# Kernel optimization log

Hardware: AMD Instinct MI355X
Metric: run time of the kernel (lower is better)

Reference implementation:

```python
import jax, jax.numpy as jnp
import numpy as np

V = 50000
E = 800000
B, FIN, FOUT, K = 2, 64, 64, 4


def setup_inputs() -> dict:
    key = jax.random.key(0)
    k1, k2, k3, k4, k5, k6 = jax.random.split(key, 6)
    inputs = jax.random.normal(k1, (B, V, FIN), dtype=jnp.float32)
    weight = jax.random.normal(k2, (K, FIN, FOUT), dtype=jnp.float32) * np.sqrt(2.0 / (FIN * K)).astype(np.float32)
    bias = jax.random.normal(k3, (FOUT,), dtype=jnp.float32)
    lap_vals = jax.random.normal(k4, (E,), dtype=jnp.float32)
    lap_rows = jax.random.randint(k5, (E,), 0, V, dtype=jnp.int32)
    lap_cols = jax.random.randint(k6, (E,), 0, V, dtype=jnp.int32)
    return {"inputs": inputs, "weight": weight, "bias": bias,
            "lap_vals": lap_vals, "lap_rows": lap_rows, "lap_cols": lap_cols}


def reference(inputs, weight, bias, lap_vals, lap_rows, lap_cols):
    B_, V_, Fin = inputs.shape
    K_, _, Fout = weight.shape

    def spmm(x):  # L @ x, L in COO; x: [V, Fin*B]
        return jax.ops.segment_sum(lap_vals[:, None] * x[lap_cols], lap_rows, num_segments=V_)

    # x0: [V, Fin*B] (Fin-major flatten, matching torch permute(1,2,0).view)
    x0 = jnp.transpose(inputs, (1, 2, 0)).reshape(V_, Fin * B_)
    xs = [x0]
    if K_ > 1:
        x1 = spmm(x0)
        xs.append(x1)
        for _ in range(2, K_):
            x2 = 2.0 * spmm(x1) - x0
            xs.append(x2)
            x0, x1 = x1, x2
    # [K,V,Fin,B] -> [B,V,Fin,K] -> [B*V, Fin*K]
    X = jnp.stack(xs).reshape(K_, V_, Fin, B_)
    X = jnp.transpose(X, (3, 1, 2, 0)).reshape(B_ * V_, Fin * K_)
    # faithful to original: weight flattened as (K*Fin, Fout)
    out = X @ weight.reshape(K_ * Fin, Fout)
    return out.reshape(B_, V_, Fout) + bias
```

## Files before the change

### kernel.cpp

```cpp
#include <hip/hip_runtime.h>
#include <hip/hip_bf16.h>


#define NV 50000
#define NE 800000
#define XROW 128
#define NROWS 100000
#define NTILES 6250
#define EPMAX 1600000
#define BSHIFT 7
#define RPB 128
#define NB 391
#define CAP 3072
#define CHUNK 4096
#define P1_BLOCKS 196
#define X0_BLOCKS 12500

using u16 = unsigned short;
using u32 = unsigned int;
using u64 = unsigned long long;
typedef __bf16 bf16x8 __attribute__((ext_vector_type(8)));
typedef float f32x4 __attribute__((ext_vector_type(4)));

__device__ __forceinline__ float bflo(u32 g) { return __uint_as_float(g << 16); }
__device__ __forceinline__ float bfhi(u32 g) { return __uint_as_float(g & 0xffff0000u); }
__device__ __forceinline__ u32 pack_bf2(float a, float b) {
    u16 ha = __builtin_bit_cast(u16, (__bf16)a);
    u16 hb = __builtin_bit_cast(u16, (__bf16)b);
    return (u32)ha | ((u32)hb << 16);
}
__device__ __forceinline__ float unpack_f16hi(u32 rec) {
    u16 h = (u16)(rec >> 16);
    return (float)__builtin_bit_cast(_Float16, h);
}
__device__ __forceinline__ int pad16(int n) { return (n + 15) & ~15; }

__global__ __launch_bounds__(256) void bin1_k(const int* __restrict__ rows, const int* __restrict__ cols,
                                              const float* __restrict__ vals,
                                              int* __restrict__ binctr, u64* __restrict__ tmp) {
    __shared__ int bcnt[NB];
    __shared__ int bofs[NB];
    __shared__ int bcur[NB];
    __shared__ int gbase[NB];
    __shared__ int ps[256];
    __shared__ u64 stage[CHUNK];
    int t = threadIdx.x;
    int base = blockIdx.x * CHUNK;
    int n = NE - base;
    if (n > CHUNK) n = CHUNK;
    if (n <= 0) return;

    for (int i = t; i < NB; i += 256) bcnt[i] = 0;
    __syncthreads();

    for (int i = t; i < n; i += 256) {
        atomicAdd(&bcnt[rows[base + i] >> BSHIFT], 1);
    }
    __syncthreads();

    int i0 = 2 * t, i1 = 2 * t + 1;
    int a0 = (i0 < NB) ? bcnt[i0] : 0;
    int a1 = (i1 < NB) ? bcnt[i1] : 0;
    ps[t] = a0 + a1;
    __syncthreads();
    for (int off = 1; off < 256; off <<= 1) {
        int v = (t >= off) ? ps[t - off] : 0;
        __syncthreads();
        ps[t] += v;
        __syncthreads();
    }
    int eb = ps[t] - (a0 + a1);
    if (i0 < NB) { bofs[i0] = eb;      bcur[i0] = eb;      gbase[i0] = i0 * CAP + atomicAdd(&binctr[i0], a0); }
    if (i1 < NB) { bofs[i1] = eb + a0; bcur[i1] = eb + a0; gbase[i1] = i1 * CAP + atomicAdd(&binctr[i1], a1); }
    __syncthreads();

    for (int i = t; i < n; i += 256) {
        int r = rows[base + i];
        int c = cols[base + i];
        u16 hv = __builtin_bit_cast(u16, (_Float16)vals[base + i]);
        u64 rec = ((u64)(u32)r << 32) | (u64)((u32)c | ((u32)hv << 16));
        int s = atomicAdd(&bcur[r >> BSHIFT], 1);
        stage[s] = rec;
    }
    __syncthreads();

    for (int i = t; i < n; i += 256) {
        u64 rec = stage[i];
        int b = (int)(rec >> (32 + BSHIFT));
        tmp[(size_t)(gbase[b] + (i - bofs[b]))] = rec;
    }
}

__global__ __launch_bounds__(256) void bcnt_k(const u64* __restrict__ tmp, const int* __restrict__ binctr,
                                              int* __restrict__ rowc, int* __restrict__ btot,
                                              int* __restrict__ done,
                                              int* __restrict__ bbase, int* __restrict__ row_ptr) {
    __shared__ int rc[RPB];
    __shared__ int rs[RPB];
    __shared__ int ps[256];
    __shared__ int flag;
    int b = blockIdx.x, t = threadIdx.x;
    int n = binctr[b];
    const u64* rec = tmp + (size_t)b * CAP;
    if (t < RPB) rc[t] = 0;
    __syncthreads();
    for (int i = t; i < n; i += 256) {
        atomicAdd(&rc[(int)(rec[i] >> 32) & (RPB - 1)], 1);
    }
    __syncthreads();
    if (t < RPB) {
        rowc[b * RPB + t] = rc[t];
        rs[t] = pad16(rc[t]);
    }
    __syncthreads();
    for (int off = 64; off > 0; off >>= 1) {
        if (t < off) rs[t] += rs[t + off];
        __syncthreads();
    }
    if (t == 0) {
        btot[b] = rs[0];
        __threadfence();
        int ticket = atomicAdd(done, 1);
        flag = (ticket == NB - 1);
    }
    __syncthreads();
    if (flag) {
        __threadfence();
        int i0 = 2 * t, i1 = 2 * t + 1;
        int a0 = (i0 < NB) ? atomicAdd(&btot[i0], 0) : 0;
        int a1 = (i1 < NB) ? atomicAdd(&btot[i1], 0) : 0;
        ps[t] = a0 + a1;
        __syncthreads();
        for (int off = 1; off < 256; off <<= 1) {
            int v = (t >= off) ? ps[t - off] : 0;
            __syncthreads();
            ps[t] += v;
            __syncthreads();
        }
        int eb = ps[t] - (a0 + a1);
        if (i0 < NB) bbase[i0] = eb;
        if (i1 < NB) bbase[i1] = eb + a0;
        if (t == 255) row_ptr[NV] = ps[255];
    }
}

__global__ __launch_bounds__(256) void place_k(const u64* __restrict__ tmp, const int* __restrict__ binctr,
                                               const int* __restrict__ rowc, const int* __restrict__ bbase,
                                               int* __restrict__ row_ptr, u32* __restrict__ epack) {
    __shared__ int rc[RPB];
    __shared__ int ro[RPB];
    int b = blockIdx.x, t = threadIdx.x;
    int n = binctr[b];
    int base = bbase[b];
    const u64* rec = tmp + (size_t)b * CAP;

    int cv = (t < RPB) ? rowc[b * RPB + t] : 0;
    int pv = pad16(cv);
    if (t < RPB) ro[t] = pv;
    __syncthreads();
    for (int off = 1; off < RPB; off <<= 1) {
        int v = 0;
        if (t < RPB && t >= off) v = ro[t - off];
        __syncthreads();
        if (t < RPB) ro[t] += v;
        __syncthreads();
    }
    if (t < RPB) {
        int ex = ro[t] - pv;
        ro[t] = ex;
        rc[t] = 0;
        int v = (b << BSHIFT) + t;
        if (v < NV) row_ptr[v] = base + ex;
    }
    __syncthreads();
    for (int i = t; i < n; i += 256) {
        u64 r64 = rec[i];
        int r = (int)(r64 >> 32) & (RPB - 1);
        int p = base + ro[r] + atomicAdd(&rc[r], 1);
        epack[p] = (u32)r64;
    }
    __syncthreads();
    if (t < RPB) {
        int s = base + ro[t] + cv;
        int e = base + ro[t] + pv;
        for (int i = s; i < e; ++i) epack[i] = 0;
    }
}

__global__ void bx0w_k(const float* __restrict__ in, u32* __restrict__ x0u,
                       const float* __restrict__ weight, u16* __restrict__ wimg) {
    int bid = blockIdx.x;
    if (bid < X0_BLOCKS) {
        int i = bid * 256 + threadIdx.x;
        int v = i >> 6, p = i & 63;
        int b = p >> 5;
        int f = (p & 31) * 2;
        const float* src = in + (size_t)b * (NV * 64) + (size_t)v * 64 + f;
        float2 t = *(const float2*)src;
        x0u[i] = pack_bf2(t.x, t.y);
    } else {
        int i = (bid - X0_BLOCKS) * 256 + threadIdx.x;
        int c = i >> 6, o = i & 63;
        int cp = ((c & 3) << 6) | (c >> 2);
        wimg[o * 264 + cp] = __builtin_bit_cast(u16, (__bf16)weight[i]);
    }
}

__global__ __launch_bounds__(256) void spmm_k(const u32* __restrict__ x,
                                              const u32* __restrict__ xprev,
                                              const int* __restrict__ row_ptr,
                                              const u32* __restrict__ epack,
                                              u32* __restrict__ xout, int mode) {
    int wave = (int)((blockIdx.x * blockDim.x + threadIdx.x) >> 6);
    u32 lane = threadIdx.x & 63;
    int row = __builtin_amdgcn_readfirstlane(wave);
    if (row >= NV) return;
    int beg = row_ptr[row];
    int end = row_ptr[row + 1];
    int q = (int)(lane >> 4);
    u32 g16 = lane & 15;

    float ax[4] = {0.f, 0.f, 0.f, 0.f};
    float ay[4] = {0.f, 0.f, 0.f, 0.f};

    for (int e = beg; e < end; e += 16) {
        uint4 r4 = *(const uint4*)(epack + e + 4 * q);
        u32 rec[4] = {r4.x, r4.y, r4.z, r4.w};
        uint4 gv[4];
        #pragma unroll
        for (int u = 0; u < 4; ++u)
            gv[u] = *(const uint4*)(x + ((rec[u] & 0xffffu) << 6) + (g16 << 2));
        #pragma unroll
        for (int u = 0; u < 4; ++u) {
            float w = unpack_f16hi(rec[u]);
            ax[0] += w * bflo(gv[u].x); ay[0] += w * bfhi(gv[u].x);
            ax[1] += w * bflo(gv[u].y); ay[1] += w * bfhi(gv[u].y);
            ax[2] += w * bflo(gv[u].z); ay[2] += w * bfhi(gv[u].z);
            ax[3] += w * bflo(gv[u].w); ay[3] += w * bfhi(gv[u].w);
        }
    }

    #pragma unroll
    for (int m = 16; m <= 32; m <<= 1) {
        #pragma unroll
        for (int j = 0; j < 4; ++j) {
            ax[j] += __shfl_xor(ax[j], m, 64);
            ay[j] += __shfl_xor(ay[j], m, 64);
        }
    }

    if (q == 0) {
        if (mode) {
            uint4 pv = *(const uint4*)(xprev + ((u32)row << 6) + (g16 << 2));
            ax[0] = 2.f * ax[0] - bflo(pv.x); ay[0] = 2.f * ay[0] - bfhi(pv.x);
            ax[1] = 2.f * ax[1] - bflo(pv.y); ay[1] = 2.f * ay[1] - bfhi(pv.y);
            ax[2] = 2.f * ax[2] - bflo(pv.z); ay[2] = 2.f * ay[2] - bfhi(pv.z);
            ax[3] = 2.f * ax[3] - bflo(pv.w); ay[3] = 2.f * ay[3] - bfhi(pv.w);
        }
        uint4 o;
        o.x = pack_bf2(ax[0], ay[0]);
        o.y = pack_bf2(ax[1], ay[1]);
        o.z = pack_bf2(ax[2], ay[2]);
        o.w = pack_bf2(ax[3], ay[3]);
        *(uint4*)(xout + ((u32)row << 6) + (g16 << 2)) = o;
    }
}

__global__ __launch_bounds__(256) void final_k(const u16* __restrict__ x_all,
                                               const u16* __restrict__ wimg,
                                               const float* __restrict__ bias,
                                               float* __restrict__ out) {
    __shared__ u16 Wt[64 * 264];
    {
        const u32* src = (const u32*)wimg;
        u32* dst = (u32*)Wt;
        #pragma unroll 4
        for (int i = threadIdx.x; i < 64 * 264 / 2; i += 256) dst[i] = src[i];
    }
    __syncthreads();

    int lane = threadIdx.x & 63;
    int wid = threadIdx.x >> 6;
    int pair = blockIdx.x * 4 + wid;
    int t0 = pair * 2;
    if (t0 >= NTILES) return;

    int m = lane & 15;
    int q8 = (lane >> 4) * 8;

    int r0 = t0 * 16 + m;
    int r1 = r0 + 16;
    const u16* arow0 = x_all + (size_t)(r0 >> 1) * XROW + (r0 & 1) * 64;
    const u16* arow1 = x_all + (size_t)(r1 >> 1) * XROW + (r1 & 1) * 64;

    f32x4 accA[4] = {{0,0,0,0},{0,0,0,0},{0,0,0,0},{0,0,0,0}};
    f32x4 accB[4] = {{0,0,0,0},{0,0,0,0},{0,0,0,0},{0,0,0,0}};

    #pragma unroll
    for (int kb = 0; kb < 8; ++kb) {
        int cb = kb * 32 + q8;
        int arr = cb >> 6;
        int f0 = cb & 63;
        size_t aoff = (size_t)arr * (NV * XROW) + f0;
        bf16x8 a0 = *(const bf16x8*)(arow0 + aoff);
        bf16x8 a1 = *(const bf16x8*)(arow1 + aoff);
        #pragma unroll
        for (int j = 0; j < 4; ++j) {
            bf16x8 bj = *(const bf16x8*)&Wt[(j * 16 + m) * 264 + kb * 32 + q8];
            accA[j] = __builtin_amdgcn_mfma_f32_16x16x32_bf16(a0, bj, accA[j], 0, 0, 0);
            accB[j] = __builtin_amdgcn_mfma_f32_16x16x32_bf16(a1, bj, accB[j], 0, 0, 0);
        }
    }

    float bv[4];
    #pragma unroll
    for (int j = 0; j < 4; ++j) bv[j] = bias[j * 16 + m];

    #pragma unroll
    for (int half = 0; half < 2; ++half) {
        int rbase = (t0 + half) * 16 + (lane >> 4) * 4;
        f32x4* acc = half ? accB : accA;
        #pragma unroll
        for (int reg = 0; reg < 4; ++reg) {
            int rr = rbase + reg;
            float* op = out + (size_t)(rr & 1) * (NV * 64) + (size_t)(rr >> 1) * 64;
            #pragma unroll
            for (int j = 0; j < 4; ++j) op[j * 16 + m] = acc[j][reg] + bv[j];
        }
    }
}

extern "C" void kernel_launch(void* const* d_in, const int* in_sizes, int n_in,
                              void* d_out, int out_size, void* d_ws, size_t ws_size,
                              hipStream_t stream) {
    const float* inputs = (const float*)d_in[0];
    const float* weight = (const float*)d_in[1];
    const float* bias   = (const float*)d_in[2];
    const float* lapv   = (const float*)d_in[3];
    const int*   lrows  = (const int*)d_in[4];
    const int*   lcols  = (const int*)d_in[5];
    float* out = (float*)d_out;

    char* ws = (char*)d_ws;
    size_t o = 0;
    auto alloc = [&](size_t bytes) -> void* {
        void* p = ws + o;
        o += (bytes + 255) & ~(size_t)255;
        return p;
    };
    u16* x_all = (u16*)alloc((size_t)4 * NV * XROW * 2);
    u32* epack = (u32*)alloc((size_t)EPMAX * 4);
    u64* tmp   = (u64*)alloc((size_t)NB * CAP * 8);
    int* row_ptr = (int*)alloc((size_t)(NV + 1) * 4);
    int* binctr  = (int*)alloc((size_t)(NB + 1) * 4);
    int* btot    = (int*)alloc((size_t)NB * 4);
    int* bbase   = (int*)alloc((size_t)NB * 4);
    int* rowc    = (int*)alloc((size_t)NB * RPB * 4);
    u16* wimg = (u16*)alloc((size_t)64 * 264 * 2);
    (void)ws_size; (void)in_sizes; (void)n_in; (void)out_size;

    int* done = binctr + NB;

    u32* x0 = (u32*)(x_all + (size_t)0 * NV * XROW);
    u32* x1 = (u32*)(x_all + (size_t)1 * NV * XROW);
    u32* x2 = (u32*)(x_all + (size_t)2 * NV * XROW);
    u32* x3 = (u32*)(x_all + (size_t)3 * NV * XROW);

    hipMemsetAsync(binctr, 0, (size_t)(NB + 1) * 4, stream);
    bin1_k<<<P1_BLOCKS, 256, 0, stream>>>(lrows, lcols, lapv, binctr, tmp);
    bcnt_k<<<NB, 256, 0, stream>>>(tmp, binctr, rowc, btot, done, bbase, row_ptr);
    place_k<<<NB, 256, 0, stream>>>(tmp, binctr, rowc, bbase, row_ptr, epack);
    bx0w_k<<<X0_BLOCKS + 64, 256, 0, stream>>>(inputs, x0, weight, wimg);

    spmm_k<<<(NV + 3) / 4, 256, 0, stream>>>(x0, nullptr, row_ptr, epack, x1, 0);
    spmm_k<<<(NV + 3) / 4, 256, 0, stream>>>(x1, x0, row_ptr, epack, x2, 1);
    spmm_k<<<(NV + 3) / 4, 256, 0, stream>>>(x2, x1, row_ptr, epack, x3, 1);

    final_k<<<(NTILES / 2 + 3) / 4, 256, 0, stream>>>(x_all, wimg, bias, out);
}
```

Baseline: 231.9 us.

## Fuse third Chebyshev SpMM with final weight GEMM into one kernel

The last sparse matmul step and the dense output projection now run in a single kernel. Each 512-thread block computes x3 for 8 vertices into a swizzled LDS tile, stages x0..x2 for the same vertices there too, and then runs MFMA against the weight image read straight from global memory. This removes one kernel launch and the write-back and re-read of x3 through HBM. In exchange, each block does only one MFMA tile with 4 waves while 4 waves sit idle. Weight fragments are now fetched from global or cache instead of LDS.

```diff
diff --git a/kernel.cpp b/kernel.cpp
--- a/kernel.cpp
+++ b/kernel.cpp
@@ -266,66 +266,104 @@
     }
 }
 
-__global__ __launch_bounds__(256) void final_k(const u16* __restrict__ x_all,
-                                               const u16* __restrict__ wimg,
-                                               const float* __restrict__ bias,
-                                               float* __restrict__ out) {
-    __shared__ u16 Wt[64 * 264];
+__global__ __launch_bounds__(512) void spmm3f_k(const u32* __restrict__ x2,
+                                                const u32* __restrict__ x1,
+                                                const int* __restrict__ row_ptr,
+                                                const u32* __restrict__ epack,
+                                                const u16* __restrict__ x_all,
+                                                const u16* __restrict__ wimg,
+                                                const float* __restrict__ bias,
+                                                float* __restrict__ out) {
+    __shared__ u32 As[4 * 8 * 64];
+    int t0 = blockIdx.x;
+    int tid = threadIdx.x;
+    int w = tid >> 6;
+    u32 lane = tid & 63;
+
+    #pragma unroll
+    for (int k = 0; k < 3; ++k) {
+        int i = tid + k * 512;
+        int arr = i >> 9;
+        int vp = (i >> 6) & 7;
+        int c = i & 63;
+        u32 val = *((const u32*)x_all + ((size_t)arr * NV + (size_t)(t0 * 8 + vp)) * 64 + c);
+        int unit = (c >> 2) ^ (vp & 7);
+        As[(arr * 8 + vp) * 64 + unit * 4 + (c & 3)] = val;
+    }
+
     {
-        const u32* src = (const u32*)wimg;
-        u32* dst = (u32*)Wt;
-        #pragma unroll 4
-        for (int i = threadIdx.x; i < 64 * 264 / 2; i += 256) dst[i] = src[i];
-    }
-    __syncthreads();
-
-    int lane = threadIdx.x & 63;
-    int wid = threadIdx.x >> 6;
-    int pair = blockIdx.x * 4 + wid;
-    int t0 = pair * 2;
-    if (t0 >= NTILES) return;
-
-    int m = lane & 15;
-    int q8 = (lane >> 4) * 8;
-
-    int r0 = t0 * 16 + m;
-    int r1 = r0 + 16;
-    const u16* arow0 = x_all + (size_t)(r0 >> 1) * XROW + (r0 & 1) * 64;
-    const u16* arow1 = x_all + (size_t)(r1 >> 1) * XROW + (r1 & 1) * 64;
-
-    f32x4 accA[4] = {{0,0,0,0},{0,0,0,0},{0,0,0,0},{0,0,0,0}};
-    f32x4 accB[4] = {{0,0,0,0},{0,0,0,0},{0,0,0,0},{0,0,0,0}};
-
-    #pragma unroll
-    for (int kb = 0; kb < 8; ++kb) {
-        int cb = kb * 32 + q8;
-        int arr = cb >> 6;
-        int f0 = cb & 63;
-        size_t aoff = (size_t)arr * (NV * XROW) + f0;
-        bf16x8 a0 = *(const bf16x8*)(arow0 + aoff);
-        bf16x8 a1 = *(const bf16x8*)(arow1 + aoff);
-        #pragma unroll
-        for (int j = 0; j < 4; ++j) {
-            bf16x8 bj = *(const bf16x8*)&Wt[(j * 16 + m) * 264 + kb * 32 + q8];
-            accA[j] = __builtin_amdgcn_mfma_f32_16x16x32_bf16(a0, bj, accA[j], 0, 0, 0);
-            accB[j] = __builtin_amdgcn_mfma_f32_16x16x32_bf16(a1, bj, accB[j], 0, 0, 0);
-        }
-    }
-
-    float bv[4];
-    #pragma unroll
-    for (int j = 0; j < 4; ++j) bv[j] = bias[j * 16 + m];
-
-    #pragma unroll
-    for (int half = 0; half < 2; ++half) {
-        int rbase = (t0 + half) * 16 + (lane >> 4) * 4;
-        f32x4* acc = half ? accB : accA;
+        int row = __builtin_amdgcn_readfirstlane(t0 * 8 + w);
+        int beg = row_ptr[row];
+        int end = row_ptr[row + 1];
+        int q = (int)(lane >> 4);
+        u32 g16 = lane & 15;
+
+        float ax[4] = {0.f, 0.f, 0.f, 0.f};
+        float ay[4] = {0.f, 0.f, 0.f, 0.f};
+
+        for (int e = beg; e < end; e += 16) {
+            uint4 r4 = *(const uint4*)(epack + e + 4 * q);
+            u32 rec[4] = {r4.x, r4.y, r4.z, r4.w};
+            uint4 gv[4];
+            #pragma unroll
+            for (int u = 0; u < 4; ++u)
+                gv[u] = *(const uint4*)(x2 + ((rec[u] & 0xffffu) << 6) + (g16 << 2));
+            #pragma unroll
+            for (int u = 0; u < 4; ++u) {
+                float wgt = unpack_f16hi(rec[u]);
+                ax[0] += wgt * bflo(gv[u].x); ay[0] += wgt * bfhi(gv[u].x);
+                ax[1] += wgt * bflo(gv[u].y); ay[1] += wgt * bfhi(gv[u].y);
+                ax[2] += wgt * bflo(gv[u].z); ay[2] += wgt * bfhi(gv[u].z);
+                ax[3] += wgt * bflo(gv[u].w); ay[3] += wgt * bfhi(gv[u].w);
+            }
+        }
+
+        #pragma unroll
+        for (int m = 16; m <= 32; m <<= 1) {
+            #pragma unroll
+            for (int j = 0; j < 4; ++j) {
+                ax[j] += __shfl_xor(ax[j], m, 64);
+                ay[j] += __shfl_xor(ay[j], m, 64);
+            }
+        }
+
+        if (q == 0) {
+            uint4 pv = *(const uint4*)(x1 + ((u32)row << 6) + (g16 << 2));
+            ax[0] = 2.f * ax[0] - bflo(pv.x); ay[0] = 2.f * ay[0] - bfhi(pv.x);
+            ax[1] = 2.f * ax[1] - bflo(pv.y); ay[1] = 2.f * ay[1] - bfhi(pv.y);
+            ax[2] = 2.f * ax[2] - bflo(pv.z); ay[2] = 2.f * ay[2] - bfhi(pv.z);
+            ax[3] = 2.f * ax[3] - bflo(pv.w); ay[3] = 2.f * ay[3] - bfhi(pv.w);
+            int unit = (int)g16 ^ (w & 7);
+            u32* dst = &As[(3 * 8 + w) * 64 + unit * 4];
+            dst[0] = pack_bf2(ax[0], ay[0]);
+            dst[1] = pack_bf2(ax[1], ay[1]);
+            dst[2] = pack_bf2(ax[2], ay[2]);
+            dst[3] = pack_bf2(ax[3], ay[3]);
+        }
+    }
+    __syncthreads();
+
+    if (w < 4) {
+        int j = w;
+        int m = (int)lane & 15;
+        int q8 = ((int)lane >> 4) * 8;
+        int vp = m >> 1;
+        int b = m & 1;
+        f32x4 acc = {0, 0, 0, 0};
+        #pragma unroll
+        for (int kb = 0; kb < 8; ++kb) {
+            int arr = kb >> 1;
+            int unit = (b * 8 + (kb & 1) * 4 + ((int)lane >> 4)) ^ (vp & 7);
+            bf16x8 a = *(const bf16x8*)&As[(arr * 8 + vp) * 64 + unit * 4];
+            bf16x8 bj = *(const bf16x8*)&wimg[(j * 16 + m) * 264 + kb * 32 + q8];
+            acc = __builtin_amdgcn_mfma_f32_16x16x32_bf16(a, bj, acc, 0, 0, 0);
+        }
+        float bv = bias[j * 16 + m];
+        int rbase = t0 * 16 + ((int)lane >> 4) * 4;
         #pragma unroll
         for (int reg = 0; reg < 4; ++reg) {
             int rr = rbase + reg;
-            float* op = out + (size_t)(rr & 1) * (NV * 64) + (size_t)(rr >> 1) * 64;
-            #pragma unroll
-            for (int j = 0; j < 4; ++j) op[j * 16 + m] = acc[j][reg] + bv[j];
+            out[(size_t)(rr & 1) * (NV * 64) + (size_t)(rr >> 1) * 64 + j * 16 + m] = acc[reg] + bv;
         }
     }
 }
@@ -364,7 +402,6 @@
     u32* x0 = (u32*)(x_all + (size_t)0 * NV * XROW);
     u32* x1 = (u32*)(x_all + (size_t)1 * NV * XROW);
     u32* x2 = (u32*)(x_all + (size_t)2 * NV * XROW);
-    u32* x3 = (u32*)(x_all + (size_t)3 * NV * XROW);
 
     hipMemsetAsync(binctr, 0, (size_t)(NB + 1) * 4, stream);
     bin1_k<<<P1_BLOCKS, 256, 0, stream>>>(lrows, lcols, lapv, binctr, tmp);
@@ -374,7 +411,6 @@
 
     spmm_k<<<(NV + 3) / 4, 256, 0, stream>>>(x0, nullptr, row_ptr, epack, x1, 0);
     spmm_k<<<(NV + 3) / 4, 256, 0, stream>>>(x1, x0, row_ptr, epack, x2, 1);
-    spmm_k<<<(NV + 3) / 4, 256, 0, stream>>>(x2, x1, row_ptr, epack, x3, 1);
-
-    final_k<<<(NTILES / 2 + 3) / 4, 256, 0, stream>>>(x_all, wimg, bias, out);
-}
+
+    spmm3f_k<<<NTILES, 512, 0, stream>>>(x2, x1, row_ptr, epack, x_all, wimg, bias, out);
+}
```

Result: no change. 227.5 us (median of 3 runs) (-1.9%).
